# Kernel optimization log

Hardware: AMD Instinct MI355X
Metric: run time of the kernel (lower is better)

Reference implementation:

```python
import jax, jax.numpy as jnp
import numpy as np

B, S, T = 128, 512, 256


def setup_inputs() -> dict:
    key = jax.random.key(0)
    k1, k2, k3, k4 = jax.random.split(key, 4)
    emissions = jax.random.normal(k1, (B, S, T), dtype=jnp.float32)
    mask = jnp.ones((B, S), dtype=bool)
    transitions = jax.random.normal(k2, (T, T), dtype=jnp.float32)
    start_transitions = jax.random.normal(k3, (T,), dtype=jnp.float32)
    end_transitions = jax.random.normal(k4, (T,), dtype=jnp.float32)
    return {
        "emissions": emissions,
        "mask": mask,
        "transitions": transitions,
        "start_transitions": start_transitions,
        "end_transitions": end_transitions,
    }


def reference(emissions, mask, transitions, start_transitions, end_transitions):
    """Batched Viterbi decode. Returns (paths [B,S] int32, best_scores [B] f32).

    Faithful to CRFLayer._viterbi_decode: score_0 = start + em_0; at each step
    next[i,j] = score[i] + trans[i,j] + em_t[j], take max/argmax over i; add
    end_transitions at the end; backtrack via backpointers. Masked (padded)
    steps carry score through unchanged with identity backpointers, so padded
    tail positions replicate the last valid tag (mask is all-ones here, so
    output equals the original's full-length paths).
    """
    Bn, Sn, Tn = emissions.shape
    ident = jnp.arange(Tn, dtype=jnp.int32)
    score0 = start_transitions[None, :] + emissions[:, 0]  # [B,T]

    em_ts = jnp.swapaxes(emissions, 0, 1)[1:]  # [S-1,B,T]
    m_ts = jnp.swapaxes(mask, 0, 1)[1:]        # [S-1,B]

    def step(score, inp):
        em_t, m_t = inp
        # nxt[b,i,j] = score[b,i] + trans[i,j] + em_t[b,j]
        nxt = score[:, :, None] + transitions[None, :, :] + em_t[:, None, :]
        best = jnp.max(nxt, axis=1)                    # [B,T]
        idx = jnp.argmax(nxt, axis=1).astype(jnp.int32)  # [B,T] best prev tag
        m = m_t[:, None]
        new_score = jnp.where(m, best, score)
        bp = jnp.where(m, idx, ident[None, :])
        return new_score, bp

    final_score, history = jax.lax.scan(step, score0, (em_ts, m_ts))  # history [S-1,B,T]
    final_score = final_score + end_transitions[None, :]
    best_scores = jnp.max(final_score, axis=1)                         # [B]
    last_tag = jnp.argmax(final_score, axis=1).astype(jnp.int32)       # [B]

    def back(tag, hist_t):
        prev = jnp.take_along_axis(hist_t, tag[:, None], axis=1)[:, 0]
        return prev, tag  # carry prev tag, emit current tag

    first_tag, tags_rest = jax.lax.scan(back, last_tag, history, reverse=True)
    # tags_rest[t] = tag at position t+1; first_tag = tag at position 0
    paths = jnp.concatenate([first_tag[:, None], jnp.swapaxes(tags_rest, 0, 1)], axis=1)
    return paths, best_scores
```

## Files before the change

### kernel.cpp

```cpp
#include <hip/hip_runtime.h>

#define Bn 128
#define Sn 512
#define Tn 256

typedef float v4f __attribute__((ext_vector_type(4)));

template <int CTRL>
__device__ __forceinline__ float dpp_fmax(float v) {
  int x = __builtin_amdgcn_mov_dpp(__float_as_int(v), CTRL, 0xF, 0xF, true);
  return fmaxf(v, __int_as_float(x));
}
__device__ __forceinline__ float row_fmax16(float v) {
  v = dpp_fmax<0x128>(v);
  v = dpp_fmax<0x124>(v);
  v = dpp_fmax<0x122>(v);
  v = dpp_fmax<0x121>(v);
  return v;
}
__device__ __forceinline__ float wave_fmax64(float v) {
  v = row_fmax16(v);
  int x = __builtin_amdgcn_ds_swizzle(__float_as_int(v), 0x401F);
  v = fmaxf(v, __int_as_float(x));
  v = fmaxf(v, __shfl_xor(v, 32));
  return v;
}
__device__ __forceinline__ float readlane_f(float v, int l) {
  return __int_as_float(__builtin_amdgcn_readlane(__float_as_int(v), l));
}

__global__ __launch_bounds__(256) void transpose_kernel(
    const float* __restrict__ tr, float* __restrict__ trT) {
  int idx = blockIdx.x * 256 + threadIdx.x;
  int i = idx >> 8;
  int j = idx & 255;
  trT[j * Tn + i] = tr[i * Tn + j];
}

__global__ __launch_bounds__(1024, 4) void viterbi_fwd(
    const float* __restrict__ em,
    const float* __restrict__ trans,
    const float* __restrict__ start,
    float* __restrict__ scores)
{
  const int b    = blockIdx.x;
  const int tid  = threadIdx.x;
  const int lane = tid & 63;
  const int w    = tid >> 6;
  const int ip   = lane >> 2;
  const int jq   = lane & 3;
  const int jbase = w * 16 + jq * 4;
  const int i0    = ip * 16;
  const int b2 = (lane >> 2) & 1;
  const int b3 = (lane >> 3) & 1;
  const int myc = jbase + b2 * 2 + b3;
  const bool writer = (lane & 48) == 0;

  __shared__ float sbuf[2][Tn];

  float4 tr[16];
#pragma unroll
  for (int k = 0; k < 16; ++k)
    tr[k] = *reinterpret_cast<const float4*>(trans + (i0 + k) * Tn + jbase);

  const float* emb = em + (size_t)b * Sn * Tn;
  float* scb = scores + (size_t)b * Sn * Tn;

  if (tid < 64) {
    int j4 = tid * 4;
    float4 st = *reinterpret_cast<const float4*>(start + j4);
    float4 e0 = *reinterpret_cast<const float4*>(emb + j4);
    float4 s0 = make_float4(st.x + e0.x, st.y + e0.y, st.z + e0.z, st.w + e0.w);
    *reinterpret_cast<float4*>(&sbuf[0][j4]) = s0;
    *reinterpret_cast<float4*>(scb + j4) = s0;
  }

  const float* em_pre = emb + 2 * Tn + myc;
  float*       sc_w   = scb + Tn + myc;
  float e_cur = 0.0f;
  if (writer) e_cur = emb[Tn + myc];
  __syncthreads();

  int cur = 0;
  for (int t = 1; t < Sn; ++t) {
    const float* sp = &sbuf[cur][i0];
    float4 a0 = *reinterpret_cast<const float4*>(sp);
    float4 a1 = *reinterpret_cast<const float4*>(sp + 4);
    float4 a2 = *reinterpret_cast<const float4*>(sp + 8);
    float4 a3 = *reinterpret_cast<const float4*>(sp + 12);

    float e_nxt = 0.0f;
    if (writer) {
      const float* p = (t + 1 < Sn) ? em_pre : em_pre - Tn;
      e_nxt = *p;
    }

    float se[16] = {a0.x,a0.y,a0.z,a0.w, a1.x,a1.y,a1.z,a1.w,
                    a2.x,a2.y,a2.z,a2.w, a3.x,a3.y,a3.z,a3.w};

    float m0 = fmaxf(fmaxf(se[0]+tr[0].x, se[1]+tr[1].x), se[2]+tr[2].x);
    float m1 = fmaxf(fmaxf(se[0]+tr[0].y, se[1]+tr[1].y), se[2]+tr[2].y);
    float m2 = fmaxf(fmaxf(se[0]+tr[0].z, se[1]+tr[1].z), se[2]+tr[2].z);
    float m3 = fmaxf(fmaxf(se[0]+tr[0].w, se[1]+tr[1].w), se[2]+tr[2].w);
#pragma unroll
    for (int k = 3; k < 15; k += 2) {
      m0 = fmaxf(fmaxf(m0, se[k]+tr[k].x), se[k+1]+tr[k+1].x);
      m1 = fmaxf(fmaxf(m1, se[k]+tr[k].y), se[k+1]+tr[k+1].y);
      m2 = fmaxf(fmaxf(m2, se[k]+tr[k].z), se[k+1]+tr[k+1].z);
      m3 = fmaxf(fmaxf(m3, se[k]+tr[k].w), se[k+1]+tr[k+1].w);
    }
    m0 = fmaxf(m0, se[15]+tr[15].x);
    m1 = fmaxf(m1, se[15]+tr[15].y);
    m2 = fmaxf(m2, se[15]+tr[15].z);
    m3 = fmaxf(m3, se[15]+tr[15].w);

    float sA = b2 ? m0 : m2;
    float rA = __shfl_xor(sA, 4);
    float sB = b2 ? m1 : m3;
    float rB = __shfl_xor(sB, 4);
    float p0 = fmaxf(b2 ? m2 : m0, rA);
    float p1 = fmaxf(b2 ? m3 : m1, rB);
    float sC = b3 ? p0 : p1;
    float rC = __shfl_xor(sC, 8);
    float q  = fmaxf(b3 ? p1 : p0, rC);
    q = fmaxf(q, __shfl_xor(q, 16));
    q = fmaxf(q, __shfl_xor(q, 32));

    if (writer) {
      float ns = q + e_cur;
      sbuf[cur ^ 1][myc] = ns;
      *sc_w = ns;
    }
    e_cur = e_nxt;
    em_pre += Tn;
    sc_w   += Tn;
    cur ^= 1;
    __syncthreads();
  }
}

__global__ __launch_bounds__(64, 1) void viterbi_bwd(
    const float* __restrict__ em,
    const float* __restrict__ trT,
    const float* __restrict__ endt,
    const float* __restrict__ scores,
    float* __restrict__ out)
{
  const int b = blockIdx.x;
  const int lane = threadIdx.x;
  const float* scb = scores + (size_t)b * Sn * Tn;
  const float* emb = em + (size_t)b * Sn * Tn;
  const int base = lane * 4;
  const int BIG = 1 << 30;

  __shared__ unsigned char pbuf[Sn];

  float warm = 0.0f;
  for (int off = base; off < Tn * Tn; off += 256) {
    float4 wv = *reinterpret_cast<const float4*>(trT + off);
    warm += wv.x + wv.y + wv.z + wv.w;
  }
  warm *= 0.0f;

  float4 s = *reinterpret_cast<const float4*>(scb + (size_t)(Sn - 1) * Tn + base);
  float4 e = *reinterpret_cast<const float4*>(endt + base);
  float d0 = (s.x + e.x) + warm;
  float d1 = (s.y + e.y) + warm;
  float d2 = (s.z + e.z) + warm;
  float d3 = (s.w + e.w) + warm;
  float bv = fmaxf(fmaxf(fmaxf(d0, d1), d2), d3);
  bv = wave_fmax64(bv);
  int li = BIG;
  if (d3 == bv) li = base + 3;
  if (d2 == bv) li = base + 2;
  if (d1 == bv) li = base + 1;
  if (d0 == bv) li = base;
  unsigned long long mk = __ballot(li != BIG);
  int tag = __shfl(li, (int)__ffsll((long long)mk) - 1);
  if (lane == 0) {
    out[Bn * Sn + b] = bv;
    pbuf[Sn - 1] = (unsigned char)tag;
  }
  tag = __builtin_amdgcn_readfirstlane(tag);

  #define LD_V4(ptr) __builtin_nontemporal_load(reinterpret_cast<const v4f*>(ptr))

  v4f S0, S1, S2, S3, E0, E1, E2, E3;
  S3 = LD_V4(scb + (size_t)(Sn - 1) * Tn + base);
  E3 = LD_V4(emb + (size_t)(Sn - 1) * Tn + base);
  S2 = LD_V4(scb + (size_t)(Sn - 2) * Tn + base);
  E2 = LD_V4(emb + (size_t)(Sn - 2) * Tn + base);
  S1 = LD_V4(scb + (size_t)(Sn - 3) * Tn + base);
  E1 = LD_V4(emb + (size_t)(Sn - 3) * Tn + base);

  #define BWD_STEP(kk_, SP_, SC_, SN_, EP_, EN_) {                           \
    const int k_ = (kk_);                                                    \
                    \
    float4 tv = *reinterpret_cast<const float4*>(trT + (size_t)tag * Tn + base); \
    __builtin_amdgcn_sched_barrier(0);                                       \
            \
    int kp_ = (k_ >= 2) ? k_ - 2 : 0;                                        \
    SN_ = LD_V4(scb + (size_t)kp_ * Tn + base);                              \
    EN_ = LD_V4(emb + (size_t)kp_ * Tn + base);                              \
    __builtin_amdgcn_sched_barrier(0);                                       \
                  \
    int comp_ = tag & 3;                                                     \
    float sPs_ = (comp_ == 0) ? SP_.x : (comp_ == 1) ? SP_.y                 \
               : (comp_ == 2) ? SP_.z : SP_.w;                               \
    float dmax_ = readlane_f(sPs_, tag >> 2);                                \
    float eVs_ = (comp_ == 0) ? EP_.x : (comp_ == 1) ? EP_.y                 \
               : (comp_ == 2) ? EP_.z : EP_.w;                               \
    float ev_ = readlane_f(eVs_, tag >> 2);                                  \
       \
    float c0_ = (SC_.x + tv.x) + ev_;                                        \
    float c1_ = (SC_.y + tv.y) + ev_;                                        \
    float c2_ = (SC_.z + tv.z) + ev_;                                        \
    float c3_ = (SC_.w + tv.w) + ev_;                                        \
    unsigned long long m0_ = __ballot(c0_ == dmax_);                         \
    unsigned long long m1_ = __ballot(c1_ == dmax_);                         \
    unsigned long long m2_ = __ballot(c2_ == dmax_);                         \
    unsigned long long m3_ = __ballot(c3_ == dmax_);                         \
    int f0_ = (int)__ffsll((long long)m0_);                                  \
    int f1_ = (int)__ffsll((long long)m1_);                                  \
    int f2_ = (int)__ffsll((long long)m2_);                                  \
    int f3_ = (int)__ffsll((long long)m3_);                                  \
    int i0_ = f0_ ? ((f0_ - 1) * 4 + 0) : BIG;                               \
    int i1_ = f1_ ? ((f1_ - 1) * 4 + 1) : BIG;                               \
    int i2_ = f2_ ? ((f2_ - 1) * 4 + 2) : BIG;                               \
    int i3_ = f3_ ? ((f3_ - 1) * 4 + 3) : BIG;                               \
    int ta_ = (i0_ < i1_) ? i0_ : i1_;                                       \
    int tb_ = (i2_ < i3_) ? i2_ : i3_;                                       \
    tag = (ta_ < tb_) ? ta_ : tb_;                                           \
    tag = __builtin_amdgcn_readfirstlane(tag);                               \
    if (lane == 0) pbuf[k_] = (unsigned char)tag;                            \
  }

  for (int kk = Sn - 2; kk >= 3; kk -= 4) {
    BWD_STEP(kk,     S3, S2, S0, E3, E0);
    BWD_STEP(kk - 1, S2, S1, S3, E2, E3);
    BWD_STEP(kk - 2, S1, S0, S2, E1, E2);
    BWD_STEP(kk - 3, S0, S3, S1, E0, E1);
  }
  BWD_STEP(2, S3, S2, S0, E3, E0);
  BWD_STEP(1, S2, S1, S3, E2, E3);
  BWD_STEP(0, S1, S0, S2, E1, E2);

  #undef BWD_STEP
  #undef LD_V4

  __syncthreads();
  for (int s2 = lane; s2 < Sn; s2 += 64)
    out[(size_t)b * Sn + s2] = (float)pbuf[s2];
}

extern "C" void kernel_launch(void* const* d_in, const int* in_sizes, int n_in,
                              void* d_out, int out_size, void* d_ws, size_t ws_size,
                              hipStream_t stream) {
  const float* em    = (const float*)d_in[0];
  const float* trans = (const float*)d_in[2];
  const float* start = (const float*)d_in[3];
  const float* endt  = (const float*)d_in[4];
  float* out = (float*)d_out;

  float* scores = (float*)d_ws;
  float* trT = (float*)((char*)d_ws + (size_t)Bn * Sn * Tn * 4);

  transpose_kernel<<<Tn * Tn / 256, 256, 0, stream>>>(trans, trT);
  viterbi_fwd<<<Bn, 1024, 0, stream>>>(em, trans, start, scores);
  viterbi_bwd<<<Bn, 64, 0, stream>>>(em, trT, endt, scores, out);
}
```

Measured before the change: 665.6 us.

## Stage backward-pass score/emission rows into LDS ring via async global-to-LDS loads

The single-wave backtrack kernel no longer keeps a short register pipeline of nontemporal global loads. It now prefetches score and emission rows into a 16-row LDS ring buffer with global_load_lds, issuing bursts of 8 rows every 8 steps, and reads the current and next rows from LDS. It also touches trT rows each burst, apparently to keep the transposed transition matrix warm in cache. The intent is to hide global latency on the serial backtrack chain. The ring reuse relies on implicit vmcnt ordering without explicit waits inside the loop, which risks reading LDS rows before their loads land.

```diff
diff --git a/kernel.cpp b/kernel.cpp
--- a/kernel.cpp
+++ b/kernel.cpp
@@ -5,6 +5,13 @@
 #define Tn 256
 
 typedef float v4f __attribute__((ext_vector_type(4)));
+
+typedef __attribute__((address_space(3))) unsigned int lds_u32_t;
+typedef __attribute__((address_space(1))) unsigned int glb_u32_t;
+
+__device__ __forceinline__ void gl_lds16(const float* g, float* l) {
+  __builtin_amdgcn_global_load_lds((const glb_u32_t*)g, (lds_u32_t*)l, 16, 0, 0);
+}
 
 template <int CTRL>
 __device__ __forceinline__ float dpp_fmax(float v) {
@@ -27,6 +34,9 @@
 }
 __device__ __forceinline__ float readlane_f(float v, int l) {
   return __int_as_float(__builtin_amdgcn_readlane(__float_as_int(v), l));
+}
+__device__ __forceinline__ float sel4(v4f v, int c) {
+  return (c == 0) ? v.x : (c == 1) ? v.y : (c == 2) ? v.z : v.w;
 }
 
 __global__ __launch_bounds__(256) void transpose_kernel(
@@ -153,6 +163,8 @@
   const int base = lane * 4;
   const int BIG = 1 << 30;
 
+  __shared__ float sc_lds[16][Tn];
+  __shared__ float em_lds[16][Tn];
   __shared__ unsigned char pbuf[Sn];
 
   float warm = 0.0f;
@@ -161,6 +173,13 @@
     warm += wv.x + wv.y + wv.z + wv.w;
   }
   warm *= 0.0f;
+
+#pragma unroll
+  for (int j = 0; j < 11; ++j) {
+    int r = (Sn - 1) - j;
+    gl_lds16(scb + (size_t)r * Tn + base, &sc_lds[r & 15][0]);
+    gl_lds16(emb + (size_t)r * Tn + base, &em_lds[r & 15][0]);
+  }
 
   float4 s = *reinterpret_cast<const float4*>(scb + (size_t)(Sn - 1) * Tn + base);
   float4 e = *reinterpret_cast<const float4*>(endt + base);
@@ -183,39 +202,46 @@
   }
   tag = __builtin_amdgcn_readfirstlane(tag);
 
-  #define LD_V4(ptr) __builtin_nontemporal_load(reinterpret_cast<const v4f*>(ptr))
-
-  v4f S0, S1, S2, S3, E0, E1, E2, E3;
-  S3 = LD_V4(scb + (size_t)(Sn - 1) * Tn + base);
-  E3 = LD_V4(emb + (size_t)(Sn - 1) * Tn + base);
-  S2 = LD_V4(scb + (size_t)(Sn - 2) * Tn + base);
-  E2 = LD_V4(emb + (size_t)(Sn - 2) * Tn + base);
-  S1 = LD_V4(scb + (size_t)(Sn - 3) * Tn + base);
-  E1 = LD_V4(emb + (size_t)(Sn - 3) * Tn + base);
-
-  #define BWD_STEP(kk_, SP_, SC_, SN_, EP_, EN_) {                           \
-    const int k_ = (kk_);                                                    \
-                    \
+  asm volatile("s_waitcnt vmcnt(0)" ::: "memory");
+  __builtin_amdgcn_sched_barrier(0);
+  v4f svP = *reinterpret_cast<const v4f*>(&sc_lds[(Sn - 1) & 15][base]);
+  v4f svC = *reinterpret_cast<const v4f*>(&sc_lds[(Sn - 2) & 15][base]);
+  v4f emP = *reinterpret_cast<const v4f*>(&em_lds[(Sn - 1) & 15][base]);
+  v4f emC = *reinterpret_cast<const v4f*>(&em_lds[(Sn - 2) & 15][base]);
+
+  #define BWD_BODY(k_, DO_BURST)  {                                          \
+            \
     float4 tv = *reinterpret_cast<const float4*>(trT + (size_t)tag * Tn + base); \
     __builtin_amdgcn_sched_barrier(0);                                       \
-            \
-    int kp_ = (k_ >= 2) ? k_ - 2 : 0;                                        \
-    SN_ = LD_V4(scb + (size_t)kp_ * Tn + base);                              \
-    EN_ = LD_V4(emb + (size_t)kp_ * Tn + base);                              \
+          \
+    int comp_ = tag & 3;                                                     \
+    float dmax_ = readlane_f(sel4(svP, comp_), tag >> 2);                    \
+    float ev_   = readlane_f(sel4(emP, comp_), tag >> 2);                    \
+                     \
+    int kn_ = (k_ > 0) ? k_ - 1 : 0;                                         \
+    v4f svN = *reinterpret_cast<const v4f*>(&sc_lds[kn_ & 15][base]);        \
+    v4f emN = *reinterpret_cast<const v4f*>(&em_lds[kn_ & 15][base]);        \
     __builtin_amdgcn_sched_barrier(0);                                       \
-                  \
-    int comp_ = tag & 3;                                                     \
-    float sPs_ = (comp_ == 0) ? SP_.x : (comp_ == 1) ? SP_.y                 \
-               : (comp_ == 2) ? SP_.z : SP_.w;                               \
-    float dmax_ = readlane_f(sPs_, tag >> 2);                                \
-    float eVs_ = (comp_ == 0) ? EP_.x : (comp_ == 1) ? EP_.y                 \
-               : (comp_ == 2) ? EP_.z : EP_.w;                               \
-    float ev_ = readlane_f(eVs_, tag >> 2);                                  \
+    if (DO_BURST) {                                                          \
+      _Pragma("unroll")                                                      \
+      for (int j_ = 0; j_ < 8; ++j_) {                                       \
+        int r_ = k_ - 10 - j_; if (r_ < 0) r_ = 0;                           \
+        gl_lds16(scb + (size_t)r_ * Tn + base, &sc_lds[r_ & 15][0]);         \
+        gl_lds16(emb + (size_t)r_ * Tn + base, &em_lds[r_ & 15][0]);         \
+      }                                                                      \
+             \
+      int gi_ = ((510 - k_) >> 3) & 31;                                      \
+      const float* tp_ = trT + gi_ * 2048 + base;                            \
+      float4 t0_ = *reinterpret_cast<const float4*>(tp_);                    \
+      float4 t1_ = *reinterpret_cast<const float4*>(tp_ + 1024);             \
+      asm volatile("" :: "v"(t0_.x), "v"(t1_.x));                            \
+    }                                                                        \
+    __builtin_amdgcn_sched_barrier(0);                                       \
        \
-    float c0_ = (SC_.x + tv.x) + ev_;                                        \
-    float c1_ = (SC_.y + tv.y) + ev_;                                        \
-    float c2_ = (SC_.z + tv.z) + ev_;                                        \
-    float c3_ = (SC_.w + tv.w) + ev_;                                        \
+    float c0_ = (svC.x + tv.x) + ev_;                                        \
+    float c1_ = (svC.y + tv.y) + ev_;                                        \
+    float c2_ = (svC.z + tv.z) + ev_;                                        \
+    float c3_ = (svC.w + tv.w) + ev_;                                        \
     unsigned long long m0_ = __ballot(c0_ == dmax_);                         \
     unsigned long long m1_ = __ballot(c1_ == dmax_);                         \
     unsigned long long m2_ = __ballot(c2_ == dmax_);                         \
@@ -233,20 +259,19 @@
     tag = (ta_ < tb_) ? ta_ : tb_;                                           \
     tag = __builtin_amdgcn_readfirstlane(tag);                               \
     if (lane == 0) pbuf[k_] = (unsigned char)tag;                            \
-  }
-
-  for (int kk = Sn - 2; kk >= 3; kk -= 4) {
-    BWD_STEP(kk,     S3, S2, S0, E3, E0);
-    BWD_STEP(kk - 1, S2, S1, S3, E2, E3);
-    BWD_STEP(kk - 2, S1, S0, S2, E1, E2);
-    BWD_STEP(kk - 3, S0, S3, S1, E0, E1);
-  }
-  BWD_STEP(2, S3, S2, S0, E3, E0);
-  BWD_STEP(1, S2, S1, S3, E2, E3);
-  BWD_STEP(0, S1, S0, S2, E1, E2);
-
-  #undef BWD_STEP
-  #undef LD_V4
+                                           \
+    svP = svC; svC = svN; emP = emC; emC = emN;                              \
+  }
+
+#pragma unroll 8
+  for (int k = Sn - 2; k >= 7; --k) {
+    BWD_BODY(k, ((k & 7) == 6 && k >= 14));
+  }
+#pragma unroll
+  for (int k = 6; k >= 0; --k) {
+    BWD_BODY(k, false);
+  }
+  #undef BWD_BODY
 
   __syncthreads();
   for (int s2 = lane; s2 < Sn; s2 += 64)
```

Measured after the change: 704.0 us. 1.06x slower.
